# Optimization experiments

Measured on AMD Instinct MI355X. Metric: run time of the kernel, lower is better.

Reference implementation:

```python
import jax, jax.numpy as jnp
import numpy as np

BOND_TOL = 0.4
CLASH_TOL = 1.5
IDEAL_CA_CA = 3.8
EPS = 1e-08


def setup_inputs() -> dict:
    key = jax.random.key(0)
    k1, _ = jax.random.split(key)
    B, L = 8, 2048
    positions = jax.random.normal(k1, (B, L, 3), dtype=jnp.float32) * 10.0
    mask = jnp.ones((B, L), dtype=jnp.float32)
    return {"positions": positions, "mask": mask}


def reference(positions, mask):
    # positions: [B, L, 3] CA coordinates; mask: [B, L]
    L = positions.shape[1]
    ca = positions
    ca_mask = mask

    # --- bond term: consecutive CA-CA distances ---
    ca_diff = ca[:, 1:] - ca[:, :-1]                       # [B, L-1, 3]
    ca_dist = jnp.sqrt(jnp.sum(ca_diff ** 2, axis=-1) + EPS)
    bond_violation = jax.nn.relu(jnp.abs(ca_dist - IDEAL_CA_CA) - BOND_TOL)
    bond_mask = ca_mask[:, 1:] * ca_mask[:, :-1]
    bond_loss = jnp.sum(bond_violation * bond_mask) / (jnp.sum(bond_mask) + EPS)

    # --- clash term: all-pairs distances, non-bonded (|i-j| > 2) ---
    all_diff = ca[:, :, None, :] - ca[:, None, :, :]       # [B, L, L, 3]
    all_dist = jnp.sqrt(jnp.sum(all_diff ** 2, axis=-1) + EPS)  # [B, L, L]
    idx = jnp.arange(L)
    seq_sep = jnp.abs(idx[None, :] - idx[:, None])         # [L, L]
    non_bonded = (seq_sep > 2).astype(ca.dtype)
    clash_violation = jax.nn.relu(CLASH_TOL - all_dist)
    pair_mask = ca_mask[:, :, None] * ca_mask[:, None, :] * non_bonded[None]
    clash_loss = jnp.sum(clash_violation * pair_mask) / (jnp.sum(pair_mask) + EPS)

    total = bond_loss + clash_loss
    # stacked: [bond_loss, clash_loss, total_violation]
    return jnp.stack([bond_loss, clash_loss, total])
```

## Files before the change

### kernel.cpp

```cpp
#include <hip/hip_runtime.h>

#define TPB 512
#define RPB 16
#define SEQ_L 2048
#define CHUNK 512
#define NCH (SEQ_L / CHUNK)
#define NBATCH 8
#define NBLOCKS 256
#define NWAVE (TPB / 64)

static constexpr float kBondTol  = 0.4f;
static constexpr float kClashTol = 1.5f;
static constexpr float kIdeal    = 3.8f;
static constexpr float kEps      = 1e-8f;
static constexpr float kThresh2  = 2.25f;

__device__ __forceinline__ float wred(float v) {
#pragma unroll
  for (int o = 32; o > 0; o >>= 1) v += __shfl_down(v, o, 64);
  return v;
}

__global__ __launch_bounds__(TPB, 2) void viol_main(
    const float* __restrict__ pos,
    const float* __restrict__ mask,
    float4* __restrict__ partial) {
  __shared__ float4 s[SEQ_L];
  __shared__ float  redm[NWAVE];
  __shared__ float  red4[NWAVE][4];

  const int b = blockIdx.x & 7;
  const int r = blockIdx.x >> 3;
  int tiles[4];
  tiles[0] = r; tiles[1] = 127 - r; tiles[2] = 63 - r; tiles[3] = 64 + r;

  const float* pb = pos  + (size_t)b * SEQ_L * 3;
  const float* mb = mask + (size_t)b * SEQ_L;

  float mpart = 0.f;
#pragma unroll
  for (int it = 0; it < SEQ_L / TPB; ++it) {
    int idx = threadIdx.x + it * TPB;
    float x = pb[3 * idx + 0];
    float y = pb[3 * idx + 1];
    float z = pb[3 * idx + 2];
    float m = mb[idx];
    s[idx] = make_float4(x, y, z, m);
    mpart += m;
  }
  mpart = wred(mpart);
  const int wid  = threadIdx.x >> 6;
  const int lane = threadIdx.x & 63;
  if (lane == 0) redm[wid] = mpart;
  __syncthreads();
  float msum = 0.f;
#pragma unroll
  for (int w = 0; w < NWAVE; ++w) msum += redm[w];

  float cv = 0.f, pm = 0.f, bv = 0.f, bm = 0.f;

  for (int tt = 0; tt < 4; ++tt) {
    const int i0 = tiles[tt] << 4;

    float px[RPB], py[RPB], pz[RPB], pw[RPB], accr[RPB];
#pragma unroll
    for (int q = 0; q < RPB; ++q) {
      float4 p = s[i0 + q];
      px[q] = p.x; py[q] = p.y; pz[q] = p.z; pw[q] = p.w;
      accr[q] = 0.f;
    }

    const int k0 = i0 >> 9;

    {
      const int j = threadIdx.x + (k0 << 9);
      const float4 pj = s[j];
#pragma unroll
      for (int q = 0; q < RPB; ++q) {
        const int i = i0 + q;
        float dx = pj.x - px[q];
        float dy = pj.y - py[q];
        float dz = pj.z - pz[q];
        float d2 = fmaf(dx, dx, fmaf(dy, dy, dz * dz));
        float dist = __builtin_amdgcn_sqrtf(d2 + kEps);
        float mw = (j > i) ? pj.w : 0.f;
        accr[q] = fmaf(fmaxf(kClashTol - dist, 0.f), mw, accr[q]);
      }
    }

#pragma unroll 2
    for (int k = k0 + 1; k < NCH; ++k) {
      float4 pj = s[threadIdx.x + (k << 9)];
      float d2r[RPB];
#pragma unroll
      for (int q = 0; q < RPB; ++q) {
        float dx = pj.x - px[q];
        float dy = pj.y - py[q];
        float dz = pj.z - pz[q];
        d2r[q] = fmaf(dx, dx, fmaf(dy, dy, dz * dz));
      }
      float mv = d2r[0];
#pragma unroll
      for (int q = 1; q < RPB; ++q) mv = fminf(mv, d2r[q]);
      if (__ballot(mv < kThresh2) != 0ull) {
#pragma unroll
        for (int q = 0; q < RPB; ++q) {
          float dist = __builtin_amdgcn_sqrtf(d2r[q] + kEps);
          accr[q] = fmaf(fmaxf(kClashTol - dist, 0.f), pj.w, accr[q]);
        }
      }
    }

#pragma unroll
    for (int q = 0; q < RPB; ++q) cv = fmaf(pw[q], accr[q], cv);
  }

  if (threadIdx.x < 64) {
    const int tile = tiles[threadIdx.x >> 4];
    const int i = (tile << 4) + (threadIdx.x & 15);
    const float4 pi = s[i];
    float nv = 0.f;
    const int jhi = (i + 2 > SEQ_L - 1) ? SEQ_L - 1 : i + 2;
    for (int j = i + 1; j <= jhi; ++j) {
      float4 pj = s[j];
      float dx = pj.x - pi.x;
      float dy = pj.y - pi.y;
      float dz = pj.z - pi.z;
      float dist = __builtin_amdgcn_sqrtf(dx * dx + dy * dy + dz * dz + kEps);
      nv += fmaxf(kClashTol - dist, 0.f) * pj.w;
    }
    cv -= pi.w * nv;

    float nm = 0.f;
    const int jlo = (i - 2 < 0) ? 0 : i - 2;
    for (int j = jlo; j <= jhi; ++j) nm += s[j].w;
    pm += pi.w * (msum - nm);

    if (i < SEQ_L - 1) {
      const float4 pj = s[i + 1];
      float dx = pj.x - pi.x;
      float dy = pj.y - pi.y;
      float dz = pj.z - pi.z;
      float dist = __builtin_amdgcn_sqrtf(dx * dx + dy * dy + dz * dz + kEps);
      float viol = fmaxf(fabsf(dist - kIdeal) - kBondTol, 0.f);
      bv += viol * pi.w * pj.w;
      bm += pi.w * pj.w;
    }
  }

  bv = wred(bv); bm = wred(bm); cv = wred(cv); pm = wred(pm);
  if (lane == 0) {
    red4[wid][0] = bv; red4[wid][1] = bm;
    red4[wid][2] = cv; red4[wid][3] = pm;
  }
  __syncthreads();
  if (threadIdx.x == 0) {
    float tbv = 0.f, tbm = 0.f, tcv = 0.f, tpm = 0.f;
#pragma unroll
    for (int w = 0; w < NWAVE; ++w) {
      tbv += red4[w][0]; tbm += red4[w][1];
      tcv += red4[w][2]; tpm += red4[w][3];
    }
    partial[blockIdx.x] = make_float4(tbv, tbm, 2.f * tcv, tpm);
  }
}

__global__ __launch_bounds__(256) void viol_reduce(
    const float4* __restrict__ partial, float* __restrict__ out) {
  __shared__ float red4[4][4];
  float4 p = partial[threadIdx.x];
  float bv = wred(p.x), bm = wred(p.y), cv = wred(p.z), pm = wred(p.w);
  const int wid  = threadIdx.x >> 6;
  const int lane = threadIdx.x & 63;
  if (lane == 0) {
    red4[wid][0] = bv; red4[wid][1] = bm;
    red4[wid][2] = cv; red4[wid][3] = pm;
  }
  __syncthreads();
  if (threadIdx.x == 0) {
    float tbv = 0.f, tbm = 0.f, tcv = 0.f, tpm = 0.f;
#pragma unroll
    for (int w = 0; w < 4; ++w) {
      tbv += red4[w][0]; tbm += red4[w][1];
      tcv += red4[w][2]; tpm += red4[w][3];
    }
    float bond  = tbv / (tbm + kEps);
    float clash = tcv / (tpm + kEps);
    out[0] = bond;
    out[1] = clash;
    out[2] = bond + clash;
  }
}

extern "C" void kernel_launch(void* const* d_in, const int* in_sizes, int n_in,
                              void* d_out, int out_size, void* d_ws, size_t ws_size,
                              hipStream_t stream) {
  const float* pos  = (const float*)d_in[0];
  const float* mask = (const float*)d_in[1];
  float* out = (float*)d_out;
  float4* partial = (float4*)d_ws;

  viol_main<<<dim3(NBLOCKS), dim3(TPB), 0, stream>>>(pos, mask, partial);
  viol_reduce<<<dim3(1), dim3(256), 0, stream>>>(partial, out);
}
```

Before: 71.43 us.

## Split work into 512 blocks of two tiles each, load only needed columns

Each block now handles two row tiles (g and 127-g) instead of four, so twice as many blocks are launched and the grid fills more CUs with better balance. Shared memory is loaded only from the first chunk the block actually needs rather than the whole sequence, and the launch bound asks for four blocks per CU. The mask sum is read straight from global memory, and the reduce kernel now loops over the larger partial array. The cost is extra per-block overhead and duplicated mask-sum work.

```diff
diff --git a/kernel.cpp b/kernel.cpp
--- a/kernel.cpp
+++ b/kernel.cpp
@@ -6,7 +6,8 @@
 #define CHUNK 512
 #define NCH (SEQ_L / CHUNK)
 #define NBATCH 8
-#define NBLOCKS 256
+#define NPAIR 64
+#define NBLOCKS (NBATCH * NPAIR)
 #define NWAVE (TPB / 64)
 
 static constexpr float kBondTol  = 0.4f;
@@ -21,7 +22,7 @@
   return v;
 }
 
-__global__ __launch_bounds__(TPB, 2) void viol_main(
+__global__ __launch_bounds__(TPB, 4) void viol_main(
     const float* __restrict__ pos,
     const float* __restrict__ mask,
     float4* __restrict__ partial) {
@@ -29,26 +30,29 @@
   __shared__ float  redm[NWAVE];
   __shared__ float  red4[NWAVE][4];
 
-  const int b = blockIdx.x & 7;
-  const int r = blockIdx.x >> 3;
-  int tiles[4];
-  tiles[0] = r; tiles[1] = 127 - r; tiles[2] = 63 - r; tiles[3] = 64 + r;
+  const int b  = blockIdx.x & 7;
+  const int g  = blockIdx.x >> 3;
+  const int i0A = g << 4;
+  const int i0B = (127 - g) << 4;
+  const int k0A = i0A >> 9;
+  const int k0B = i0B >> 9;
+  const int jbase = k0A << 9;
 
   const float* pb = pos  + (size_t)b * SEQ_L * 3;
   const float* mb = mask + (size_t)b * SEQ_L;
 
   float mpart = 0.f;
 #pragma unroll
-  for (int it = 0; it < SEQ_L / TPB; ++it) {
-    int idx = threadIdx.x + it * TPB;
+  for (int it = 0; it < NCH; ++it) mpart += mb[threadIdx.x + (it << 9)];
+  mpart = wred(mpart);
+
+  for (int idx = jbase + (int)threadIdx.x; idx < SEQ_L; idx += TPB) {
     float x = pb[3 * idx + 0];
     float y = pb[3 * idx + 1];
     float z = pb[3 * idx + 2];
-    float m = mb[idx];
-    s[idx] = make_float4(x, y, z, m);
-    mpart += m;
-  }
-  mpart = wred(mpart);
+    s[idx] = make_float4(x, y, z, mb[idx]);
+  }
+
   const int wid  = threadIdx.x >> 6;
   const int lane = threadIdx.x & 63;
   if (lane == 0) redm[wid] = mpart;
@@ -59,8 +63,10 @@
 
   float cv = 0.f, pm = 0.f, bv = 0.f, bm = 0.f;
 
-  for (int tt = 0; tt < 4; ++tt) {
-    const int i0 = tiles[tt] << 4;
+#pragma unroll
+  for (int tt = 0; tt < 2; ++tt) {
+    const int i0 = tt ? i0B : i0A;
+    const int k0 = tt ? k0B : k0A;
 
     float px[RPB], py[RPB], pz[RPB], pw[RPB], accr[RPB];
 #pragma unroll
@@ -70,10 +76,8 @@
       accr[q] = 0.f;
     }
 
-    const int k0 = i0 >> 9;
-
     {
-      const int j = threadIdx.x + (k0 << 9);
+      const int j = (int)threadIdx.x + (k0 << 9);
       const float4 pj = s[j];
 #pragma unroll
       for (int q = 0; q < RPB; ++q) {
@@ -88,7 +92,6 @@
       }
     }
 
-#pragma unroll 2
     for (int k = k0 + 1; k < NCH; ++k) {
       float4 pj = s[threadIdx.x + (k << 9)];
       float d2r[RPB];
@@ -115,9 +118,8 @@
     for (int q = 0; q < RPB; ++q) cv = fmaf(pw[q], accr[q], cv);
   }
 
-  if (threadIdx.x < 64) {
-    const int tile = tiles[threadIdx.x >> 4];
-    const int i = (tile << 4) + (threadIdx.x & 15);
+  if (threadIdx.x < 32) {
+    const int i = ((threadIdx.x & 16) ? i0B : i0A) + (int)(threadIdx.x & 15);
     const float4 pi = s[i];
     float nv = 0.f;
     const int jhi = (i + 2 > SEQ_L - 1) ? SEQ_L - 1 : i + 2;
@@ -133,7 +135,7 @@
 
     float nm = 0.f;
     const int jlo = (i - 2 < 0) ? 0 : i - 2;
-    for (int j = jlo; j <= jhi; ++j) nm += s[j].w;
+    for (int j = jlo; j <= jhi; ++j) nm += mb[j];
     pm += pi.w * (msum - nm);
 
     if (i < SEQ_L - 1) {
@@ -168,8 +170,13 @@
 __global__ __launch_bounds__(256) void viol_reduce(
     const float4* __restrict__ partial, float* __restrict__ out) {
   __shared__ float red4[4][4];
-  float4 p = partial[threadIdx.x];
-  float bv = wred(p.x), bm = wred(p.y), cv = wred(p.z), pm = wred(p.w);
+  float bv = 0.f, bm = 0.f, cv = 0.f, pm = 0.f;
+#pragma unroll
+  for (int i = threadIdx.x; i < NBLOCKS; i += 256) {
+    float4 p = partial[i];
+    bv += p.x; bm += p.y; cv += p.z; pm += p.w;
+  }
+  bv = wred(bv); bm = wred(bm); cv = wred(cv); pm = wred(pm);
   const int wid  = threadIdx.x >> 6;
   const int lane = threadIdx.x & 63;
   if (lane == 0) {
```

Result: slower. 73.29 us (+2.6%).
